# Performance work log

Hardware: AMD Instinct MI355X
Metric: run time of the kernel (lower is better)

## Reference

```python
import jax, jax.numpy as jnp
import numpy as np

BATCH, SEQ, HIDDEN = 4, 4096, 2880
NUM_EXPERTS, TOP_K = 128, 4


def setup_inputs() -> dict:
    key = jax.random.key(0)
    k1, k2, k3, k4, k5 = jax.random.split(key, 5)
    hidden_states = jax.random.normal(k1, (BATCH, SEQ, HIDDEN), dtype=jnp.float32)
    modality_mask = jax.random.randint(k2, (BATCH, SEQ), 0, 2) == 1  # True = vision token
    weight = jax.random.normal(k3, (NUM_EXPERTS, HIDDEN), dtype=jnp.float32) * 0.02
    bias = jax.random.normal(k4, (NUM_EXPERTS,), dtype=jnp.float32) * 0.02
    vision_bias = jax.random.normal(k5, (NUM_EXPERTS,), dtype=jnp.float32) * 0.02
    return {
        "hidden_states": hidden_states,
        "modality_mask": modality_mask,
        "weight": weight,
        "bias": bias,
        "vision_bias": vision_bias,
    }


def reference(hidden_states, modality_mask, weight, bias, vision_bias):
    # Flatten tokens: (num_tokens, hidden_dim)
    x = hidden_states.reshape(-1, hidden_states.shape[-1])
    mm = modality_mask.reshape(-1)  # (num_tokens,) bool

    # router_logits = x @ W^T + b, then add vision bias only for vision tokens
    logits = jnp.einsum("td,ed->te", x, weight) + bias  # (T, E)
    logits = logits + jnp.where(mm[:, None], vision_bias.astype(logits.dtype), 0.0)

    # top-k over experts, softmax over the selected k logits
    top_vals, top_idx = jax.lax.top_k(logits, TOP_K)      # (T, k)
    top_probs = jax.nn.softmax(top_vals, axis=-1)

    # scatter normalized probs back into a dense (T, E) score matrix
    T = logits.shape[0]
    rows = jnp.arange(T)[:, None]
    router_scores = jnp.zeros_like(logits).at[rows, top_idx].set(top_probs)
    return router_scores, top_idx
```

## Files before the change

### kernel.cpp

```cpp
#include <hip/hip_runtime.h>

constexpr int T_TOK = 16384;
constexpr int NEXP  = 128;
constexpr int HID   = 2880;
constexpr int TOPK  = 4;

constexpr int KSPLIT = 6;
constexpr int KS     = HID / KSPLIT;
constexpr int BM     = 128;
constexpr int BK     = 32;
constexpr int NIT    = KS / BK;
constexpr int WELEMS = NEXP * HID;

typedef __attribute__((ext_vector_type(8))) short bf16x8;
typedef __attribute__((ext_vector_type(4))) float f32x4;

__device__ inline void split3(float f, unsigned& hb, unsigned& mb, unsigned& lb) {
    unsigned u = __float_as_uint(f);
    unsigned rne = u + 0x7FFFu + ((u >> 16) & 1u);
    hb = rne & 0xFFFF0000u;
    float r = f - __uint_as_float(hb);
    mb = __float_as_uint(r) & 0xFFFF0000u;
    lb = __float_as_uint(r - __uint_as_float(mb));
}

__global__ __launch_bounds__(256)
void w_split_kernel(const float* __restrict__ w, unsigned short* __restrict__ wh,
                    unsigned short* __restrict__ wm, unsigned short* __restrict__ wl) {
    int i = blockIdx.x * 256 + threadIdx.x;
    if (i < WELEMS) {
        unsigned hb, mb, lb;
        split3(w[i], hb, mb, lb);
        wh[i] = (unsigned short)(hb >> 16);
        wm[i] = (unsigned short)(mb >> 16);
        wl[i] = (unsigned short)(lb >> 16);
    }
}

__global__ __launch_bounds__(256, 2)
void gemm_mfma(const float* __restrict__ x,
               const unsigned short* __restrict__ wh,
               const unsigned short* __restrict__ wm,
               const unsigned short* __restrict__ wl,
               float* __restrict__ part) {
    __shared__ unsigned short bs[3 * NEXP * BK];

    const int tid  = threadIdx.x;
    const int wv   = tid >> 6;
    const int lane = tid & 63;
    const int lm   = lane & 15;
    const int lq   = lane >> 4;

    const int tile   = blockIdx.x / KSPLIT;
    const int split  = blockIdx.x % KSPLIT;
    const int k_base = split * KS;

    f32x4 acc[2][8];
#pragma unroll
    for (int i = 0; i < 2; ++i)
#pragma unroll
        for (int j = 0; j < 8; ++j) acc[i][j] = (f32x4){0.f, 0.f, 0.f, 0.f};

    const float* xb = x + (size_t)tile * BM * HID + k_base;

    for (int it = 0; it < NIT; ++it) {
        const int k0 = k_base + it * BK;
#pragma unroll
        for (int r = 0; r < 6; ++r) {
            const int c  = r * 256 + wv * 64 + lane;
            const int cc = c & 511;
            const int e  = cc >> 2;
            const int kq = (cc & 3) << 3;
            const unsigned short* plane = (r < 2) ? wh : (r < 4) ? wm : wl;
            const unsigned short* src = plane + (size_t)e * HID + k0 + kq;
            __builtin_amdgcn_global_load_lds(
                (const __attribute__((address_space(1))) void*)src,
                (__attribute__((address_space(3))) void*)&bs[c * 8], 16, 0, 0);
        }

        unsigned ah[2][4], am[2][4], al[2][4];
#pragma unroll
        for (int i = 0; i < 2; ++i) {
            const float* ap =
                xb + (size_t)(wv * 32 + i * 16 + lm) * HID + it * BK + lq * 8;
            float4 a0 = *reinterpret_cast<const float4*>(ap);
            float4 a1 = *reinterpret_cast<const float4*>(ap + 4);
            float fv[8] = {a0.x, a0.y, a0.z, a0.w, a1.x, a1.y, a1.z, a1.w};
            unsigned hb[8], mb[8], lb[8];
#pragma unroll
            for (int e2 = 0; e2 < 8; ++e2) split3(fv[e2], hb[e2], mb[e2], lb[e2]);
#pragma unroll
            for (int p = 0; p < 4; ++p) {
                ah[i][p] = __builtin_amdgcn_perm(hb[2*p+1], hb[2*p], 0x07060302u);
                am[i][p] = __builtin_amdgcn_perm(mb[2*p+1], mb[2*p], 0x07060302u);
                al[i][p] = __builtin_amdgcn_perm(lb[2*p+1], lb[2*p], 0x07060302u);
            }
        }
        __syncthreads();

#pragma unroll
        for (int j = 0; j < 8; ++j) {
            const int boff = (j * 16 + lm) * BK + lq * 8;
            bf16x8 Bh = *reinterpret_cast<const bf16x8*>(&bs[boff]);
            bf16x8 Bm = *reinterpret_cast<const bf16x8*>(&bs[NEXP * BK + boff]);
            bf16x8 Bl = *reinterpret_cast<const bf16x8*>(&bs[2 * NEXP * BK + boff]);
#pragma unroll
            for (int i = 0; i < 2; ++i) {
                union { unsigned u[4]; bf16x8 v; } Ah, Am, Al;
#pragma unroll
                for (int p = 0; p < 4; ++p) {
                    Ah.u[p] = ah[i][p]; Am.u[p] = am[i][p]; Al.u[p] = al[i][p];
                }
                acc[i][j] = __builtin_amdgcn_mfma_f32_16x16x32_bf16(Ah.v, Bh, acc[i][j], 0, 0, 0);
                acc[i][j] = __builtin_amdgcn_mfma_f32_16x16x32_bf16(Ah.v, Bm, acc[i][j], 0, 0, 0);
                acc[i][j] = __builtin_amdgcn_mfma_f32_16x16x32_bf16(Am.v, Bh, acc[i][j], 0, 0, 0);
                acc[i][j] = __builtin_amdgcn_mfma_f32_16x16x32_bf16(Am.v, Bm, acc[i][j], 0, 0, 0);
                acc[i][j] = __builtin_amdgcn_mfma_f32_16x16x32_bf16(Ah.v, Bl, acc[i][j], 0, 0, 0);
                acc[i][j] = __builtin_amdgcn_mfma_f32_16x16x32_bf16(Al.v, Bh, acc[i][j], 0, 0, 0);
            }
        }
        __syncthreads();
    }

#pragma unroll
    for (int i = 0; i < 2; ++i) {
        const int trow = tile * BM + wv * 32 + i * 16 + lq * 4;
#pragma unroll
        for (int j = 0; j < 8; ++j) {
            const int e = j * 16 + lm;
            float* p = part + ((size_t)split * T_TOK + trow) * NEXP + e;
#pragma unroll
            for (int r = 0; r < 4; ++r) p[(size_t)r * NEXP] = acc[i][j][r];
        }
    }
}

__global__ __launch_bounds__(256)
void topk_scatter(const float* __restrict__ part, const int* __restrict__ mm,
                  const float* __restrict__ bias, const float* __restrict__ vbias,
                  float* __restrict__ out) {
    const int lane = threadIdx.x & 63;
    const int wid  = threadIdx.x >> 6;
    const int t    = blockIdx.x * 4 + wid;

    const int e0 = lane, e1 = 64 + lane;
    float v0 = bias[e0];
    float v1 = bias[e1];
    if (mm[t] != 0) { v0 += vbias[e0]; v1 += vbias[e1]; }
#pragma unroll
    for (int s = 0; s < KSPLIT; ++s) {
        const float* p = part + ((size_t)s * T_TOK + t) * NEXP;
        v0 += p[e0];
        v1 += p[e1];
    }

    float lv0 = v0, lv1 = v1;
    float tv[TOPK];
    int   ti[TOPK];
#pragma unroll
    for (int k = 0; k < TOPK; ++k) {
        float bv; int bi;
        if (lv0 >= lv1) { bv = lv0; bi = e0; }
        else            { bv = lv1; bi = e1; }
#pragma unroll
        for (int off = 32; off >= 1; off >>= 1) {
            float ov = __shfl_xor(bv, off, 64);
            int   oi = __shfl_xor(bi, off, 64);
            if (ov > bv || (ov == bv && oi < bi)) { bv = ov; bi = oi; }
        }
        tv[k] = bv;
        ti[k] = bi;
        if (bi == e0) lv0 = -__builtin_inff();
        if (bi == e1) lv1 = -__builtin_inff();
    }

    const float m = tv[0];
    float ex[TOPK], s = 0.f;
#pragma unroll
    for (int k = 0; k < TOPK; ++k) { ex[k] = expf(tv[k] - m); s += ex[k]; }
    const float inv = 1.0f / s;

    float s0 = 0.f, s1 = 0.f;
#pragma unroll
    for (int k = 0; k < TOPK; ++k) {
        const float p = ex[k] * inv;
        if (ti[k] == e0) s0 = p;
        if (ti[k] == e1) s1 = p;
    }
    out[(size_t)t * NEXP + e0] = s0;
    out[(size_t)t * NEXP + e1] = s1;
    if (lane < TOPK)
        out[(size_t)T_TOK * NEXP + (size_t)t * TOPK + lane] = (float)ti[lane];
}

extern "C" void kernel_launch(void* const* d_in, const int* in_sizes, int n_in,
                              void* d_out, int out_size, void* d_ws, size_t ws_size,
                              hipStream_t stream) {
    const float* x     = (const float*)d_in[0];
    const int*   mm    = (const int*)d_in[1];
    const float* w     = (const float*)d_in[2];
    const float* bias  = (const float*)d_in[3];
    const float* vbias = (const float*)d_in[4];
    float* out  = (float*)d_out;

    float* part = (float*)d_ws;
    const size_t part_bytes = (size_t)KSPLIT * T_TOK * NEXP * sizeof(float);
    unsigned short* whp = (unsigned short*)((char*)d_ws + part_bytes);
    unsigned short* wmp = whp + WELEMS;
    unsigned short* wlp = wmp + WELEMS;

    hipLaunchKernelGGL(w_split_kernel, dim3((WELEMS + 255) / 256), dim3(256), 0,
                       stream, w, whp, wmp, wlp);
    hipLaunchKernelGGL(gemm_mfma, dim3((T_TOK / BM) * KSPLIT), dim3(256), 0, stream,
                       x, whp, wmp, wlp, part);
    hipLaunchKernelGGL(topk_scatter, dim3(T_TOK / 4), dim3(256), 0, stream,
                       part, mm, bias, vbias, out);
}
```

Before: 311.2 us.

## Double-buffer weight tiles and prefetch activations with uneven K-split of eight

Adds a second LDS buffer for the three bf16 weight planes so the next K chunk's global-to-LDS loads are issued before computing on the current chunk. Activation loads for the next iteration are prefetched into registers after the current chunk has been split. This collapses two barriers per iteration into one. KSPLIT rises from 6 to 8, with uneven chunk ranges, which raises grid parallelism but also adds partial-sum traffic. LDS use doubles, which may limit occupancy, and the workspace holding the partial sums grows.

```diff
diff --git a/kernel.cpp b/kernel.cpp
--- a/kernel.cpp
+++ b/kernel.cpp
@@ -5,11 +5,10 @@
 constexpr int HID   = 2880;
 constexpr int TOPK  = 4;
 
-constexpr int KSPLIT = 6;
-constexpr int KS     = HID / KSPLIT;
+constexpr int KSPLIT = 8;
+constexpr int KCH    = HID / 32;
 constexpr int BM     = 128;
 constexpr int BK     = 32;
-constexpr int NIT    = KS / BK;
 constexpr int WELEMS = NEXP * HID;
 
 typedef __attribute__((ext_vector_type(8))) short bf16x8;
@@ -43,7 +42,7 @@
                const unsigned short* __restrict__ wm,
                const unsigned short* __restrict__ wl,
                float* __restrict__ part) {
-    __shared__ unsigned short bs[3 * NEXP * BK];
+    __shared__ unsigned short bs[2][3 * NEXP * BK];
 
     const int tid  = threadIdx.x;
     const int wv   = tid >> 6;
@@ -51,9 +50,10 @@
     const int lm   = lane & 15;
     const int lq   = lane >> 4;
 
-    const int tile   = blockIdx.x / KSPLIT;
-    const int split  = blockIdx.x % KSPLIT;
-    const int k_base = split * KS;
+    const int tile  = blockIdx.x / KSPLIT;
+    const int split = blockIdx.x % KSPLIT;
+    const int kcb   = (KCH * split) / KSPLIT;
+    const int nit   = (KCH * (split + 1)) / KSPLIT - kcb;
 
     f32x4 acc[2][8];
 #pragma unroll
@@ -61,13 +61,13 @@
 #pragma unroll
         for (int j = 0; j < 8; ++j) acc[i][j] = (f32x4){0.f, 0.f, 0.f, 0.f};
 
-    const float* xb = x + (size_t)tile * BM * HID + k_base;
-
-    for (int it = 0; it < NIT; ++it) {
-        const int k0 = k_base + it * BK;
+    const float* xb = x + (size_t)tile * BM * HID;
+
+    auto stage = [&](int it, int buf) {
+        const int k0 = (kcb + it) * 32;
 #pragma unroll
         for (int r = 0; r < 6; ++r) {
-            const int c  = r * 256 + wv * 64 + lane;
+            const int c  = (r * 4 + wv) * 64 + lane;
             const int cc = c & 511;
             const int e  = cc >> 2;
             const int kq = (cc & 3) << 3;
@@ -75,17 +75,33 @@
             const unsigned short* src = plane + (size_t)e * HID + k0 + kq;
             __builtin_amdgcn_global_load_lds(
                 (const __attribute__((address_space(1))) void*)src,
-                (__attribute__((address_space(3))) void*)&bs[c * 8], 16, 0, 0);
-        }
+                (__attribute__((address_space(3))) void*)&bs[buf][c * 8], 16, 0, 0);
+        }
+    };
+    auto loadx = [&](int it, float4 xr[2][2]) {
+        const int k0 = (kcb + it) * 32;
+#pragma unroll
+        for (int i = 0; i < 2; ++i) {
+            const float* ap = xb + (size_t)(wv * 32 + i * 16 + lm) * HID + k0 + lq * 8;
+            xr[i][0] = *reinterpret_cast<const float4*>(ap);
+            xr[i][1] = *reinterpret_cast<const float4*>(ap + 4);
+        }
+    };
+
+    float4 xr[2][2];
+    stage(0, 0);
+    loadx(0, xr);
+
+    for (int it = 0; it < nit; ++it) {
+        const int cur = it & 1;
+        __syncthreads();
+        if (it + 1 < nit) stage(it + 1, cur ^ 1);
 
         unsigned ah[2][4], am[2][4], al[2][4];
 #pragma unroll
         for (int i = 0; i < 2; ++i) {
-            const float* ap =
-                xb + (size_t)(wv * 32 + i * 16 + lm) * HID + it * BK + lq * 8;
-            float4 a0 = *reinterpret_cast<const float4*>(ap);
-            float4 a1 = *reinterpret_cast<const float4*>(ap + 4);
-            float fv[8] = {a0.x, a0.y, a0.z, a0.w, a1.x, a1.y, a1.z, a1.w};
+            float fv[8] = {xr[i][0].x, xr[i][0].y, xr[i][0].z, xr[i][0].w,
+                           xr[i][1].x, xr[i][1].y, xr[i][1].z, xr[i][1].w};
             unsigned hb[8], mb[8], lb[8];
 #pragma unroll
             for (int e2 = 0; e2 < 8; ++e2) split3(fv[e2], hb[e2], mb[e2], lb[e2]);
@@ -96,14 +112,14 @@
                 al[i][p] = __builtin_amdgcn_perm(lb[2*p+1], lb[2*p], 0x07060302u);
             }
         }
-        __syncthreads();
+        if (it + 1 < nit) loadx(it + 1, xr);
 
 #pragma unroll
         for (int j = 0; j < 8; ++j) {
             const int boff = (j * 16 + lm) * BK + lq * 8;
-            bf16x8 Bh = *reinterpret_cast<const bf16x8*>(&bs[boff]);
-            bf16x8 Bm = *reinterpret_cast<const bf16x8*>(&bs[NEXP * BK + boff]);
-            bf16x8 Bl = *reinterpret_cast<const bf16x8*>(&bs[2 * NEXP * BK + boff]);
+            bf16x8 Bh = *reinterpret_cast<const bf16x8*>(&bs[cur][boff]);
+            bf16x8 Bm = *reinterpret_cast<const bf16x8*>(&bs[cur][NEXP * BK + boff]);
+            bf16x8 Bl = *reinterpret_cast<const bf16x8*>(&bs[cur][2 * NEXP * BK + boff]);
 #pragma unroll
             for (int i = 0; i < 2; ++i) {
                 union { unsigned u[4]; bf16x8 v; } Ah, Am, Al;
@@ -119,7 +135,6 @@
                 acc[i][j] = __builtin_amdgcn_mfma_f32_16x16x32_bf16(Al.v, Bh, acc[i][j], 0, 0, 0);
             }
         }
-        __syncthreads();
     }
 
 #pragma unroll
```

New measurement: 310.1 us. No clear change (-0.4%).
